# Optimization experiments

Measured on AMD Instinct MI355X. Metric: run time of the kernel, lower is better.

Reference implementation:

```python
import jax, jax.numpy as jnp
import numpy as np
import math

S, B, D, H = 2048, 4, 1024, 16
DH = D // H

def setup_inputs() -> dict:
    key = jax.random.key(0)
    ks = jax.random.split(key, 6)
    x = jax.random.normal(ks[0], (S, B, D), dtype=jnp.float32)
    # causal additive mask (finite large negative for numerical safety)
    i = jnp.arange(S)
    attn_mask = jnp.where(i[None, :] > i[:, None], jnp.float32(-1e9), jnp.float32(0.0))
    beta = jnp.zeros((H,), dtype=jnp.float32)  # per-head log-scale, init 0 -> exp=1
    xav = math.sqrt(6.0 / (D + D))  # xavier_uniform bound
    Wq = jax.random.uniform(ks[1], (D, D), minval=-xav, maxval=xav, dtype=jnp.float32)
    Wk = jax.random.uniform(ks[2], (D, D), minval=-xav, maxval=xav, dtype=jnp.float32)
    Wv = jax.random.uniform(ks[3], (D, D), minval=-xav, maxval=xav, dtype=jnp.float32)
    Wo = jax.random.uniform(ks[4], (D, D), minval=-xav, maxval=xav, dtype=jnp.float32)
    z = jnp.zeros((D,), dtype=jnp.float32)
    return {"x": x, "attn_mask": attn_mask, "beta": beta,
            "Wq": Wq, "bq": z, "Wk": Wk, "bk": z, "Wv": Wv, "bv": z, "Wo": Wo, "bo": z}

def reference(x, attn_mask, beta, Wq, bq, Wk, bk, Wv, bv, Wo, bo):
    s, b, d = x.shape
    h, dh = H, DH
    q = x @ Wq.T + bq  # (s, b, d)
    k = x @ Wk.T + bk
    v = x @ Wv.T + bv
    # attn_sink: append zero key/value token, pad mask with a zero column
    k = jnp.concatenate([k, jnp.zeros((1, b, d), k.dtype)], axis=0)  # (s+1, b, d)
    v = jnp.concatenate([v, jnp.zeros((1, b, d), v.dtype)], axis=0)
    mask = jnp.pad(attn_mask, ((0, 0), (0, 1)))  # (s, s+1)
    t = s + 1
    # split heads: (seq, b, h, dh) -> (b, h, seq, dh)
    qh = q.reshape(s, b, h, dh).transpose(1, 2, 0, 3)
    kh = k.reshape(t, b, h, dh).transpose(1, 2, 0, 3)
    vh = v.reshape(t, b, h, dh).transpose(1, 2, 0, 3)
    scale = (jnp.exp(beta) * math.sqrt(dh))[None, :, None, None]
    qh = qh / scale
    scores = jnp.einsum('bhsd,bhtd->bhst', qh, kh) + mask[None, None]
    w = jax.nn.softmax(scores, axis=-1)
    out = jnp.einsum('bhst,bhtd->bhsd', w, vh)  # (b, h, s, dh)
    out = out.transpose(2, 0, 1, 3).reshape(s, b, d)
    return out @ Wo.T + bo
```

## Files before the change

### kernel.cpp

```cpp
#include <hip/hip_runtime.h>
#include <hip/hip_bf16.h>
#include <math.h>

#define S_LEN   2048
#define BATCH   4
#define DMODEL  1024
#define NHEAD   16
#define DHEAD   64
#define MROWS   (S_LEN * BATCH)

typedef __bf16 bf16;
typedef __bf16 bf16x8 __attribute__((ext_vector_type(8)));
typedef __bf16 bf16x4 __attribute__((ext_vector_type(4)));
typedef short  short4_t __attribute__((ext_vector_type(4)));
typedef float  f32x4  __attribute__((ext_vector_type(4)));

#define LOG2E 1.4426950408889634f

#define AS1C(p) (const __attribute__((address_space(1))) void*)(p)
#define AS3(p)  (__attribute__((address_space(3))) void*)(p)


__global__ __launch_bounds__(256) void cast_all(const float* __restrict__ x,
                                                const float* __restrict__ wq,
                                                const float* __restrict__ wk,
                                                const float* __restrict__ wv,
                                                const float* __restrict__ wo,
                                                bf16* __restrict__ xb,
                                                bf16* __restrict__ wqkv,
                                                bf16* __restrict__ wob) {
    const int i = blockIdx.x * 256 + threadIdx.x;
    constexpr int NX8 = MROWS * DMODEL / 8;
    constexpr int NW8 = DMODEL * DMODEL / 8;
    const float* src;
    bf16* dst;
    int k;
    if (i < NX8) {
        src = x; dst = xb; k = i;
    } else {
        const int j   = i - NX8;
        const int seg = j >> 17;
        k = j & (NW8 - 1);
        if (seg == 0)      { src = wq; dst = wqkv; }
        else if (seg == 1) { src = wk; dst = wqkv + (size_t)DMODEL * DMODEL; }
        else if (seg == 2) { src = wv; dst = wqkv + (size_t)2 * DMODEL * DMODEL; }
        else               { src = wo; dst = wob; }
    }
    const float4* p = (const float4*)src;
    float4 a = p[(size_t)k * 2], b = p[(size_t)k * 2 + 1];
    bf16x8 o;
    o[0] = (bf16)a.x; o[1] = (bf16)a.y; o[2] = (bf16)a.z; o[3] = (bf16)a.w;
    o[4] = (bf16)b.x; o[5] = (bf16)b.y; o[6] = (bf16)b.z; o[7] = (bf16)b.w;
    *(bf16x8*)(dst + (size_t)k * 8) = o;
}

__global__ __launch_bounds__(512, 6) void qkv_gemm(const bf16* __restrict__ A,
                                                   const bf16* __restrict__ W,
                                                   const float* __restrict__ bq,
                                                   const float* __restrict__ bk,
                                                   const float* __restrict__ bv,
                                                   const float* __restrict__ beta,
                                                   bf16* __restrict__ Qo,
                                                   bf16* __restrict__ Kp,
                                                   bf16* __restrict__ Vp) {
    constexpr int BK = 32;
    constexpr int NT = DMODEL / BK;
    __shared__ __align__(16) bf16 sA[3][128 * BK];
    __shared__ __align__(16) bf16 sB[3][128 * BK];
    const int t    = threadIdx.x;
    const int lane = t & 63;
    const int wave = t >> 6;
    const int wr   = wave >> 2;
    const int wc   = wave & 3;
    const int lq   = lane & 15;
    const int lg   = lane >> 4;
    const int bn   = blockIdx.x * 128;
    const int bm   = blockIdx.y * 128;

    const int schunk = (lane & 3) ^ ((lane >> 3) & 3);
    const bf16* ApS = A + (size_t)(bm + wave * 16 + (lane >> 2)) * DMODEL + schunk * 8;
    const bf16* WpS = W + (size_t)(bn + wave * 16 + (lane >> 2)) * DMODEL + schunk * 8;
    const int koff = (lg ^ ((lq >> 1) & 3)) * 8;
    f32x4 acc[4][2] = {};

#define QSTG(si_, ko_)                                                                   \
    __builtin_amdgcn_global_load_lds(AS1C(ApS + (ko_)), AS3(&sA[si_][wave * 512]), 16, 0, 0); \
    __builtin_amdgcn_global_load_lds(AS1C(WpS + (ko_)), AS3(&sB[si_][wave * 512]), 16, 0, 0);

    QSTG(0, 0)
    QSTG(1, BK)
    asm volatile("s_waitcnt vmcnt(2)\n\ts_barrier" ::: "memory");

    int bi = 0, si = 2, st = 2;
    for (int tt = 0; tt < NT; ++tt) {
        QSTG(si, (size_t)st * BK)
        const bf16* At = sA[bi];
        const bf16* Bt = sB[bi];
        bf16x8 bf0 = *(const bf16x8*)&Bt[(wc * 32 +      lq) * BK + koff];
        bf16x8 bf1 = *(const bf16x8*)&Bt[(wc * 32 + 16 + lq) * BK + koff];
        bf16x8 af[4];
#pragma unroll
        for (int mt = 0; mt < 4; mt++)
            af[mt] = *(const bf16x8*)&At[(wr * 64 + mt * 16 + lq) * BK + koff];
        __builtin_amdgcn_s_setprio(1);
#pragma unroll
        for (int mt = 0; mt < 4; mt++) {
            acc[mt][0] = __builtin_amdgcn_mfma_f32_16x16x32_bf16(af[mt], bf0, acc[mt][0], 0, 0, 0);
            acc[mt][1] = __builtin_amdgcn_mfma_f32_16x16x32_bf16(af[mt], bf1, acc[mt][1], 0, 0, 0);
        }
        __builtin_amdgcn_s_setprio(0);
        asm volatile("s_waitcnt vmcnt(2)\n\ts_barrier" ::: "memory");
        bi = (bi == 2) ? 0 : bi + 1;
        si = (si == 2) ? 0 : si + 1;
        st = (st == NT - 1) ? 0 : st + 1;
    }
#undef QSTG

    const int seg = blockIdx.x >> 3;
    const int bnl = (blockIdx.x & 7) * 128;
    const float* bias = (seg == 0) ? bq : (seg == 1) ? bk : bv;

    if (seg == 0) {
#pragma unroll
        for (int nt = 0; nt < 2; nt++) {
            const int col = bnl + wc * 32 + nt * 16 + lq;
            const float bvv = bias[col];
            const float sc = LOG2E / (__expf(beta[col >> 6]) * 8.0f);
#pragma unroll
            for (int mt = 0; mt < 4; mt++) {
                const int row = bm + wr * 64 + mt * 16 + lg * 4;
#pragma unroll
                for (int r = 0; r < 4; r++) {
                    float v = (acc[mt][nt][r] + bvv) * sc;
                    Qo[(size_t)(row + r) * DMODEL + col] = (bf16)v;
                }
            }
        }
    } else {
        bf16* out = (seg == 1) ? Kp : Vp;
#pragma unroll
        for (int mt = 0; mt < 4; mt++) {
            const int F   = bm + wr * 64 + mt * 16;
            const int S0X = F >> 2;
            const int T   = S0X >> 4;
            const int sl  = (S0X & 15) + lg;
#pragma unroll
            for (int nt = 0; nt < 2; nt++) {
                const int col = bnl + wc * 32 + nt * 16 + lq;
                const int h   = col >> 6;
                const int dh  = col & 63;
                const float bvv = bias[col];
#pragma unroll
                for (int r = 0; r < 4; r++) {
                    float v = acc[mt][nt][r] + bvv;
                    size_t addr;
                    if (seg == 1) {
                        addr = ((size_t)((r * 16 + h) * 128 + T)) * 1024
                             + (dh >> 5) * 512
                             + (sl + 16 * ((dh >> 3) & 3)) * 8
                             + (dh & 7);
                    } else {
                        addr = ((size_t)((r * 16 + h) * 128 + T)) * 1024
                             + (dh >> 4) * 256 + ((dh & 15) + 16 * (sl >> 2)) * 4
                             + (sl & 3);
                    }
                    out[addr] = (bf16)v;
                }
            }
        }
    }
}

__global__ __launch_bounds__(256, 3) void gemm_out(const bf16* __restrict__ A,
                                                   const bf16* __restrict__ W,
                                                   const float* __restrict__ bias,
                                                   float* __restrict__ C) {
    constexpr int BK = 32;
    constexpr int NTILES = DMODEL / BK;
    __shared__ __align__(16) bf16 sA[3][128 * BK];
    __shared__ __align__(16) bf16 sB[3][128 * BK];

    const int t    = threadIdx.x;
    const int lane = t & 63;
    const int wave = t >> 6;
    const int wr   = wave >> 1;
    const int wc   = wave & 1;
    const int lq   = lane & 15;
    const int lg   = lane >> 4;

    const int bid = (int)blockIdx.x + 8 * (int)blockIdx.y;
    const int swz = (bid & 7) * 64 + (bid >> 3);
    const int bn  = (swz & 7) * 128;
    const int bm  = (swz >> 3) * 128;

    const int schunk = (lane & 3) ^ ((lane >> 3) & 3);
    const bf16* ApS = A + (size_t)(bm + wave * 32 + (lane >> 2)) * DMODEL + schunk * 8;
    const bf16* WpS = W + (size_t)(bn + wave * 32 + (lane >> 2)) * DMODEL + schunk * 8;
    const int koff = (lg ^ ((lq >> 1) & 3)) * 8;

    f32x4 acc[4][4] = {};

#define OSTAGE(si_, ko_)                                                                              \
    __builtin_amdgcn_global_load_lds(AS1C(ApS + (ko_)),               AS3(&sA[si_][(wave*32 +  0)*BK]), 16,0,0); \
    __builtin_amdgcn_global_load_lds(AS1C(ApS + 16*DMODEL + (ko_)),   AS3(&sA[si_][(wave*32 + 16)*BK]), 16,0,0); \
    __builtin_amdgcn_global_load_lds(AS1C(WpS + (ko_)),               AS3(&sB[si_][(wave*32 +  0)*BK]), 16,0,0); \
    __builtin_amdgcn_global_load_lds(AS1C(WpS + 16*DMODEL + (ko_)),   AS3(&sB[si_][(wave*32 + 16)*BK]), 16,0,0);

    OSTAGE(0, 0)
    OSTAGE(1, BK)
    asm volatile("s_waitcnt vmcnt(4)\n\ts_barrier" ::: "memory");

    int bi = 0, si = 2, st = 2;
    for (int tt = 0; tt < NTILES; ++tt) {
        OSTAGE(si, (size_t)st * BK)
        const bf16* At = sA[bi];
        const bf16* Bt = sB[bi];
        bf16x8 bfr[4], af[4];
#pragma unroll
        for (int nt = 0; nt < 4; nt++)
            bfr[nt] = *(const bf16x8*)&Bt[(wc * 64 + nt * 16 + lq) * BK + koff];
#pragma unroll
        for (int mt = 0; mt < 4; mt++)
            af[mt] = *(const bf16x8*)&At[(wr * 64 + mt * 16 + lq) * BK + koff];
        __builtin_amdgcn_s_setprio(1);
#pragma unroll
        for (int mt = 0; mt < 4; mt++)
#pragma unroll
            for (int nt = 0; nt < 4; nt++)
                acc[mt][nt] = __builtin_amdgcn_mfma_f32_16x16x32_bf16(af[mt], bfr[nt], acc[mt][nt], 0, 0, 0);
        __builtin_amdgcn_s_setprio(0);
        asm volatile("s_waitcnt vmcnt(4)\n\ts_barrier" ::: "memory");
        bi = (bi == 2) ? 0 : bi + 1;
        si = (si == 2) ? 0 : si + 1;
        st = (st == NTILES - 1) ? 0 : st + 1;
    }
#undef OSTAGE

#pragma unroll
    for (int nt = 0; nt < 4; nt++) {
        const int col = bn + wc * 64 + nt * 16 + lq;
        const float bvv = bias[col];
#pragma unroll
        for (int mt = 0; mt < 4; mt++) {
            const int row = bm + wr * 64 + mt * 16 + lg * 4;
#pragma unroll
            for (int r = 0; r < 4; r++)
                C[(size_t)(row + r) * DMODEL + col] = acc[mt][nt][r] + bvv;
        }
    }
}

__global__ __launch_bounds__(256, 3) void attn_kernel(const bf16* __restrict__ Q,
                                                      const bf16* __restrict__ Kp,
                                                      const bf16* __restrict__ Vp,
                                                      bf16* __restrict__ O) {
    __shared__ __align__(16) float sO[64 * 65];
    __shared__ __align__(16) float sL[256];

    const int t    = threadIdx.x;
    const int lane = t & 63;
    const int wave = t >> 6;
    const int lq = lane & 15;
    const int lg = lane >> 4;

    const int bid = (int)blockIdx.x + 16 * ((int)blockIdx.y + 16 * (int)blockIdx.z);
    const int swz = (bid & 7) * 128 + (bid >> 3);
    const int idx = swz & 15;
    const int h   = (swz >> 4) & 15;
    const int b   = swz >> 8;

    const bf16* Kb = Kp + (size_t)(b * NHEAD + h) * 131072;
    const bf16* Vb = Vp + (size_t)(b * NHEAD + h) * 131072;

#pragma clang loop unroll(disable)
    for (int pass = 0; pass < 2; ++pass) {
        const int qi = (pass == 0) ? (31 - idx) : idx;
        const int qb = qi * 64;

        bf16x8 qf[4][2];
#pragma unroll
        for (int nt = 0; nt < 4; nt++)
#pragma unroll
            for (int kc = 0; kc < 2; kc++)
                qf[nt][kc] = *(const bf16x8*)
                    &Q[((size_t)(qb + nt * 16 + lq) * BATCH + b) * DMODEL + h * DHEAD + kc * 32 + lg * 8];

        f32x4 o_acc[4][4] = {};
        float l_lane[4] = {0.f, 0.f, 0.f, 0.f};

        bf16x8 kc0 = *(const bf16x8*)(Kb + (size_t)wave * 1024 + lane * 8);
        bf16x8 kc1 = *(const bf16x8*)(Kb + (size_t)wave * 1024 + 512 + lane * 8);
        bf16x4 vc0 = *(const bf16x4*)(Vb + (size_t)wave * 1024 +   0 + lane * 4);
        bf16x4 vc1 = *(const bf16x4*)(Vb + (size_t)wave * 1024 + 256 + lane * 4);
        bf16x4 vc2 = *(const bf16x4*)(Vb + (size_t)wave * 1024 + 512 + lane * 4);
        bf16x4 vc3 = *(const bf16x4*)(Vb + (size_t)wave * 1024 + 768 + lane * 4);

        for (int kt = 0; kt <= qi; kt++) {
            const int tn = ((kt < qi) ? (kt + 1) : 0) * 4 + wave;
            const bf16* Kn = Kb + (size_t)tn * 1024;
            const bf16* Vn = Vb + (size_t)tn * 1024;
            bf16x8 kn0 = *(const bf16x8*)(Kn + lane * 8);
            bf16x8 kn1 = *(const bf16x8*)(Kn + 512 + lane * 8);
            bf16x4 vn0 = *(const bf16x4*)(Vn +   0 + lane * 4);
            bf16x4 vn1 = *(const bf16x4*)(Vn + 256 + lane * 4);
            bf16x4 vn2 = *(const bf16x4*)(Vn + 512 + lane * 4);
            bf16x4 vn3 = *(const bf16x4*)(Vn + 768 + lane * 4);

            f32x4 st[4];
            __builtin_amdgcn_s_setprio(1);
#pragma unroll
            for (int nt = 0; nt < 4; nt++) {
                f32x4 a = {};
                a = __builtin_amdgcn_mfma_f32_16x16x32_bf16(kc0, qf[nt][0], a, 0, 0, 0);
                a = __builtin_amdgcn_mfma_f32_16x16x32_bf16(kc1, qf[nt][1], a, 0, 0, 0);
                st[nt] = a;
            }
            __builtin_amdgcn_s_setprio(0);

            if (kt == qi) {
#pragma unroll
                for (int nt = 0; nt < 4; nt++)
#pragma unroll
                    for (int r = 0; r < 4; r++)
                        if (wave * 16 + lg * 4 + r > nt * 16 + lq) st[nt][r] = -1e30f;
            }

            short4_t pf[4];
#pragma unroll
            for (int nt = 0; nt < 4; nt++) {
                float p0 = __builtin_amdgcn_exp2f(st[nt][0]);
                float p1 = __builtin_amdgcn_exp2f(st[nt][1]);
                float p2 = __builtin_amdgcn_exp2f(st[nt][2]);
                float p3 = __builtin_amdgcn_exp2f(st[nt][3]);
                l_lane[nt] += (p0 + p1) + (p2 + p3);
                bf16x4 pv;
                pv[0] = (bf16)p0; pv[1] = (bf16)p1; pv[2] = (bf16)p2; pv[3] = (bf16)p3;
                pf[nt] = __builtin_bit_cast(short4_t, pv);
            }

            short4_t va0 = __builtin_bit_cast(short4_t, vc0);
            short4_t va1 = __builtin_bit_cast(short4_t, vc1);
            short4_t va2 = __builtin_bit_cast(short4_t, vc2);
            short4_t va3 = __builtin_bit_cast(short4_t, vc3);
            __builtin_amdgcn_s_setprio(1);
#pragma unroll
            for (int nt = 0; nt < 4; nt++) {
                o_acc[0][nt] = __builtin_amdgcn_mfma_f32_16x16x16bf16_1k(va0, pf[nt], o_acc[0][nt], 0, 0, 0);
                o_acc[1][nt] = __builtin_amdgcn_mfma_f32_16x16x16bf16_1k(va1, pf[nt], o_acc[1][nt], 0, 0, 0);
                o_acc[2][nt] = __builtin_amdgcn_mfma_f32_16x16x16bf16_1k(va2, pf[nt], o_acc[2][nt], 0, 0, 0);
                o_acc[3][nt] = __builtin_amdgcn_mfma_f32_16x16x16bf16_1k(va3, pf[nt], o_acc[3][nt], 0, 0, 0);
            }
            __builtin_amdgcn_s_setprio(0);

            kc0 = kn0; kc1 = kn1;
            vc0 = vn0; vc1 = vn1; vc2 = vn2; vc3 = vn3;
        }

#pragma unroll
        for (int nt = 0; nt < 4; nt++) {
            float v = l_lane[nt];
            v += __shfl_xor(v, 16);
            v += __shfl_xor(v, 32);
            if (lg == 0) sL[wave * 64 + nt * 16 + lq] = v;
        }

#pragma unroll
        for (int rd = 0; rd < 4; rd++) {
#pragma unroll
            for (int dtc = 0; dtc < 4; dtc++) {
                if (((wave + rd) & 3) == dtc) {
                    if (rd == 0) {
#pragma unroll
                        for (int nt = 0; nt < 4; nt++)
#pragma unroll
                            for (int r = 0; r < 4; r++)
                                sO[(dtc * 16 + lg * 4 + r) * 65 + nt * 16 + lq] = o_acc[dtc][nt][r];
                    } else {
#pragma unroll
                        for (int nt = 0; nt < 4; nt++)
#pragma unroll
                            for (int r = 0; r < 4; r++)
                                sO[(dtc * 16 + lg * 4 + r) * 65 + nt * 16 + lq] += o_acc[dtc][nt][r];
                    }
                }
            }
            __syncthreads();
        }

        const int dt = wave;
        float rec[4];
#pragma unroll
        for (int nt = 0; nt < 4; nt++) {
            float lt = 1.0f + sL[nt * 16 + lq] + sL[64 + nt * 16 + lq]
                     + sL[128 + nt * 16 + lq] + sL[192 + nt * 16 + lq];
            rec[nt] = 1.0f / lt;
        }
#pragma unroll
        for (int nt = 0; nt < 4; nt++) {
            bf16x4 ov;
#pragma unroll
            for (int r = 0; r < 4; r++)
                ov[r] = (bf16)(sO[(dt * 16 + lg * 4 + r) * 65 + nt * 16 + lq] * rec[nt]);
            *(bf16x4*)&O[((size_t)(qb + nt * 16 + lq) * BATCH + b) * DMODEL + h * DHEAD + dt * 16 + lg * 4] = ov;
        }

        __syncthreads();
    }
}

extern "C" void kernel_launch(void* const* d_in, const int* in_sizes, int n_in,
                              void* d_out, int out_size, void* d_ws, size_t ws_size,
                              hipStream_t stream) {
    const float* x    = (const float*)d_in[0];
    const float* beta = (const float*)d_in[2];
    const float* Wq   = (const float*)d_in[3];
    const float* bq   = (const float*)d_in[4];
    const float* Wk   = (const float*)d_in[5];
    const float* bk   = (const float*)d_in[6];
    const float* Wv   = (const float*)d_in[7];
    const float* bv   = (const float*)d_in[8];
    const float* Wo   = (const float*)d_in[9];
    const float* bo   = (const float*)d_in[10];
    float* out = (float*)d_out;

    char* ws = (char*)d_ws;
    size_t off = 0;
    auto alloc = [&](size_t bytes) -> void* {
        void* p = ws + off;
        off += (bytes + 255) & ~(size_t)255;
        return p;
    };
    const size_t xbytes = (size_t)MROWS * DMODEL * sizeof(bf16);
    const size_t wbytes = (size_t)DMODEL * DMODEL * sizeof(bf16);
    bf16* xb   = (bf16*)alloc(xbytes);
    bf16* wqkv = (bf16*)alloc(3 * wbytes);
    bf16* wob  = (bf16*)alloc(wbytes);
    bf16* qws  = (bf16*)alloc(xbytes);
    bf16* kpb  = (bf16*)alloc(xbytes);
    bf16* vpb  = (bf16*)alloc(xbytes);
    bf16* aob  = (bf16*)alloc(xbytes);

    constexpr int NX8 = MROWS * DMODEL / 8;
    constexpr int NW8 = DMODEL * DMODEL / 8;
    cast_all<<<(NX8 + 4 * NW8) / 256, 256, 0, stream>>>(x, Wq, Wk, Wv, Wo, xb, wqkv, wob);

    dim3 qgrid(3 * DMODEL / 128, MROWS / 128);
    qkv_gemm<<<qgrid, 512, 0, stream>>>(xb, wqkv, bq, bk, bv, beta, qws, kpb, vpb);

    dim3 agrid(S_LEN / 128, NHEAD, BATCH);
    attn_kernel<<<agrid, 256, 0, stream>>>(qws, kpb, vpb, aob);

    dim3 ogrid(DMODEL / 128, MROWS / 128);
    gemm_out<<<ogrid, 256, 0, stream>>>(aob, wob, bo, out);
}
```

Before: 274.7 us.

## Split attention into one query tile per block and stage Q in LDS

```diff
diff --git a/kernel.cpp b/kernel.cpp
--- a/kernel.cpp
+++ b/kernel.cpp
@@ -250,12 +250,13 @@
     }
 }
 
-__global__ __launch_bounds__(256, 3) void attn_kernel(const bf16* __restrict__ Q,
+__global__ __launch_bounds__(256, 4) void attn_kernel(const bf16* __restrict__ Q,
                                                       const bf16* __restrict__ Kp,
                                                       const bf16* __restrict__ Vp,
                                                       bf16* __restrict__ O) {
     __shared__ __align__(16) float sO[64 * 65];
     __shared__ __align__(16) float sL[256];
+    __shared__ __align__(16) bf16  sQ[4096];
 
     const int t    = threadIdx.x;
     const int lane = t & 63;
@@ -263,148 +264,149 @@
     const int lq = lane & 15;
     const int lg = lane >> 4;
 
-    const int bid = (int)blockIdx.x + 16 * ((int)blockIdx.y + 16 * (int)blockIdx.z);
-    const int swz = (bid & 7) * 128 + (bid >> 3);
-    const int idx = swz & 15;
-    const int h   = (swz >> 4) & 15;
-    const int b   = swz >> 8;
+    const int bid = (int)blockIdx.x + 32 * ((int)blockIdx.y + 16 * (int)blockIdx.z);
+    const int swz = (bid & 7) * 256 + (bid >> 3);
+    const int qi  = 31 - (swz & 31);
+    const int h   = (swz >> 5) & 15;
+    const int b   = swz >> 9;
+    const int qb  = qi * 64;
 
     const bf16* Kb = Kp + (size_t)(b * NHEAD + h) * 131072;
     const bf16* Vb = Vp + (size_t)(b * NHEAD + h) * 131072;
 
-#pragma clang loop unroll(disable)
-    for (int pass = 0; pass < 2; ++pass) {
-        const int qi = (pass == 0) ? (31 - idx) : idx;
-        const int qb = qi * 64;
-
-        bf16x8 qf[4][2];
-#pragma unroll
-        for (int nt = 0; nt < 4; nt++)
-#pragma unroll
-            for (int kc = 0; kc < 2; kc++)
-                qf[nt][kc] = *(const bf16x8*)
-                    &Q[((size_t)(qb + nt * 16 + lq) * BATCH + b) * DMODEL + h * DHEAD + kc * 32 + lg * 8];
-
-        f32x4 o_acc[4][4] = {};
-        float l_lane[4] = {0.f, 0.f, 0.f, 0.f};
-
-        bf16x8 kc0 = *(const bf16x8*)(Kb + (size_t)wave * 1024 + lane * 8);
-        bf16x8 kc1 = *(const bf16x8*)(Kb + (size_t)wave * 1024 + 512 + lane * 8);
-        bf16x4 vc0 = *(const bf16x4*)(Vb + (size_t)wave * 1024 +   0 + lane * 4);
-        bf16x4 vc1 = *(const bf16x4*)(Vb + (size_t)wave * 1024 + 256 + lane * 4);
-        bf16x4 vc2 = *(const bf16x4*)(Vb + (size_t)wave * 1024 + 512 + lane * 4);
-        bf16x4 vc3 = *(const bf16x4*)(Vb + (size_t)wave * 1024 + 768 + lane * 4);
-
-        for (int kt = 0; kt <= qi; kt++) {
-            const int tn = ((kt < qi) ? (kt + 1) : 0) * 4 + wave;
-            const bf16* Kn = Kb + (size_t)tn * 1024;
-            const bf16* Vn = Vb + (size_t)tn * 1024;
-            bf16x8 kn0 = *(const bf16x8*)(Kn + lane * 8);
-            bf16x8 kn1 = *(const bf16x8*)(Kn + 512 + lane * 8);
-            bf16x4 vn0 = *(const bf16x4*)(Vn +   0 + lane * 4);
-            bf16x4 vn1 = *(const bf16x4*)(Vn + 256 + lane * 4);
-            bf16x4 vn2 = *(const bf16x4*)(Vn + 512 + lane * 4);
-            bf16x4 vn3 = *(const bf16x4*)(Vn + 768 + lane * 4);
-
-            f32x4 st[4];
-            __builtin_amdgcn_s_setprio(1);
-#pragma unroll
-            for (int nt = 0; nt < 4; nt++) {
-                f32x4 a = {};
-                a = __builtin_amdgcn_mfma_f32_16x16x32_bf16(kc0, qf[nt][0], a, 0, 0, 0);
-                a = __builtin_amdgcn_mfma_f32_16x16x32_bf16(kc1, qf[nt][1], a, 0, 0, 0);
-                st[nt] = a;
-            }
-            __builtin_amdgcn_s_setprio(0);
-
-            if (kt == qi) {
-#pragma unroll
-                for (int nt = 0; nt < 4; nt++)
-#pragma unroll
-                    for (int r = 0; r < 4; r++)
-                        if (wave * 16 + lg * 4 + r > nt * 16 + lq) st[nt][r] = -1e30f;
-            }
-
-            short4_t pf[4];
-#pragma unroll
-            for (int nt = 0; nt < 4; nt++) {
-                float p0 = __builtin_amdgcn_exp2f(st[nt][0]);
-                float p1 = __builtin_amdgcn_exp2f(st[nt][1]);
-                float p2 = __builtin_amdgcn_exp2f(st[nt][2]);
-                float p3 = __builtin_amdgcn_exp2f(st[nt][3]);
-                l_lane[nt] += (p0 + p1) + (p2 + p3);
-                bf16x4 pv;
-                pv[0] = (bf16)p0; pv[1] = (bf16)p1; pv[2] = (bf16)p2; pv[3] = (bf16)p3;
-                pf[nt] = __builtin_bit_cast(short4_t, pv);
-            }
-
-            short4_t va0 = __builtin_bit_cast(short4_t, vc0);
-            short4_t va1 = __builtin_bit_cast(short4_t, vc1);
-            short4_t va2 = __builtin_bit_cast(short4_t, vc2);
-            short4_t va3 = __builtin_bit_cast(short4_t, vc3);
-            __builtin_amdgcn_s_setprio(1);
-#pragma unroll
-            for (int nt = 0; nt < 4; nt++) {
-                o_acc[0][nt] = __builtin_amdgcn_mfma_f32_16x16x16bf16_1k(va0, pf[nt], o_acc[0][nt], 0, 0, 0);
-                o_acc[1][nt] = __builtin_amdgcn_mfma_f32_16x16x16bf16_1k(va1, pf[nt], o_acc[1][nt], 0, 0, 0);
-                o_acc[2][nt] = __builtin_amdgcn_mfma_f32_16x16x16bf16_1k(va2, pf[nt], o_acc[2][nt], 0, 0, 0);
-                o_acc[3][nt] = __builtin_amdgcn_mfma_f32_16x16x16bf16_1k(va3, pf[nt], o_acc[3][nt], 0, 0, 0);
-            }
-            __builtin_amdgcn_s_setprio(0);
-
-            kc0 = kn0; kc1 = kn1;
-            vc0 = vn0; vc1 = vn1; vc2 = vn2; vc3 = vn3;
-        }
-
+    {
+        const int rw  = wave * 8 + (lane >> 3);
+        const int lch = (lane & 7) ^ (lane >> 3);
+        const bf16* q0 = Q + ((size_t)(qb + rw) * BATCH + b) * DMODEL + h * DHEAD + lch * 8;
+        const bf16* q1 = Q + ((size_t)(qb + 32 + rw) * BATCH + b) * DMODEL + h * DHEAD + lch * 8;
+        __builtin_amdgcn_global_load_lds(AS1C(q0), AS3(&sQ[wave * 512]),        16, 0, 0);
+        __builtin_amdgcn_global_load_lds(AS1C(q1), AS3(&sQ[2048 + wave * 512]), 16, 0, 0);
+    }
+
+    const int a0 = lq * 64 + ((0 + lg) ^ (lq & 7)) * 8;
+    const int a1 = lq * 64 + ((4 + lg) ^ (lq & 7)) * 8;
+
+    f32x4 o_acc[4][4] = {};
+    float l_lane[4] = {0.f, 0.f, 0.f, 0.f};
+
+    bf16x8 kc0 = *(const bf16x8*)(Kb + (size_t)wave * 1024 + lane * 8);
+    bf16x8 kc1 = *(const bf16x8*)(Kb + (size_t)wave * 1024 + 512 + lane * 8);
+    bf16x4 vc0 = *(const bf16x4*)(Vb + (size_t)wave * 1024 +   0 + lane * 4);
+    bf16x4 vc1 = *(const bf16x4*)(Vb + (size_t)wave * 1024 + 256 + lane * 4);
+    bf16x4 vc2 = *(const bf16x4*)(Vb + (size_t)wave * 1024 + 512 + lane * 4);
+    bf16x4 vc3 = *(const bf16x4*)(Vb + (size_t)wave * 1024 + 768 + lane * 4);
+
+    asm volatile("s_waitcnt vmcnt(0)\n\ts_barrier" ::: "memory");
+
+    for (int kt = 0; kt <= qi; kt++) {
+        const int tn = ((kt < qi) ? (kt + 1) : 0) * 4 + wave;
+        const bf16* Kn = Kb + (size_t)tn * 1024;
+        const bf16* Vn = Vb + (size_t)tn * 1024;
+        bf16x8 kn0 = *(const bf16x8*)(Kn + lane * 8);
+        bf16x8 kn1 = *(const bf16x8*)(Kn + 512 + lane * 8);
+        bf16x4 vn0 = *(const bf16x4*)(Vn +   0 + lane * 4);
+        bf16x4 vn1 = *(const bf16x4*)(Vn + 256 + lane * 4);
+        bf16x4 vn2 = *(const bf16x4*)(Vn + 512 + lane * 4);
+        bf16x4 vn3 = *(const bf16x4*)(Vn + 768 + lane * 4);
+
+        f32x4 st[4];
+        __builtin_amdgcn_s_setprio(1);
 #pragma unroll
         for (int nt = 0; nt < 4; nt++) {
-            float v = l_lane[nt];
-            v += __shfl_xor(v, 16);
-            v += __shfl_xor(v, 32);
-            if (lg == 0) sL[wave * 64 + nt * 16 + lq] = v;
-        }
-
-#pragma unroll
-        for (int rd = 0; rd < 4; rd++) {
-#pragma unroll
-            for (int dtc = 0; dtc < 4; dtc++) {
-                if (((wave + rd) & 3) == dtc) {
-                    if (rd == 0) {
-#pragma unroll
-                        for (int nt = 0; nt < 4; nt++)
-#pragma unroll
-                            for (int r = 0; r < 4; r++)
-                                sO[(dtc * 16 + lg * 4 + r) * 65 + nt * 16 + lq] = o_acc[dtc][nt][r];
-                    } else {
-#pragma unroll
-                        for (int nt = 0; nt < 4; nt++)
-#pragma unroll
-                            for (int r = 0; r < 4; r++)
-                                sO[(dtc * 16 + lg * 4 + r) * 65 + nt * 16 + lq] += o_acc[dtc][nt][r];
-                    }
+            bf16x8 q0 = *(const bf16x8*)&sQ[nt * 1024 + a0];
+            bf16x8 q1 = *(const bf16x8*)&sQ[nt * 1024 + a1];
+            f32x4 a = {};
+            a = __builtin_amdgcn_mfma_f32_16x16x32_bf16(kc0, q0, a, 0, 0, 0);
+            a = __builtin_amdgcn_mfma_f32_16x16x32_bf16(kc1, q1, a, 0, 0, 0);
+            st[nt] = a;
+        }
+        __builtin_amdgcn_s_setprio(0);
+
+        if (kt == qi) {
+#pragma unroll
+            for (int nt = 0; nt < 4; nt++)
+#pragma unroll
+                for (int r = 0; r < 4; r++)
+                    if (wave * 16 + lg * 4 + r > nt * 16 + lq) st[nt][r] = -1e30f;
+        }
+
+        short4_t pf[4];
+#pragma unroll
+        for (int nt = 0; nt < 4; nt++) {
+            float p0 = __builtin_amdgcn_exp2f(st[nt][0]);
+            float p1 = __builtin_amdgcn_exp2f(st[nt][1]);
+            float p2 = __builtin_amdgcn_exp2f(st[nt][2]);
+            float p3 = __builtin_amdgcn_exp2f(st[nt][3]);
+            l_lane[nt] += (p0 + p1) + (p2 + p3);
+            bf16x4 pv;
+            pv[0] = (bf16)p0; pv[1] = (bf16)p1; pv[2] = (bf16)p2; pv[3] = (bf16)p3;
+            pf[nt] = __builtin_bit_cast(short4_t, pv);
+        }
+
+        short4_t va0 = __builtin_bit_cast(short4_t, vc0);
+        short4_t va1 = __builtin_bit_cast(short4_t, vc1);
+        short4_t va2 = __builtin_bit_cast(short4_t, vc2);
+        short4_t va3 = __builtin_bit_cast(short4_t, vc3);
+        __builtin_amdgcn_s_setprio(1);
+#pragma unroll
+        for (int nt = 0; nt < 4; nt++) {
+            o_acc[0][nt] = __builtin_amdgcn_mfma_f32_16x16x16bf16_1k(va0, pf[nt], o_acc[0][nt], 0, 0, 0);
+            o_acc[1][nt] = __builtin_amdgcn_mfma_f32_16x16x16bf16_1k(va1, pf[nt], o_acc[1][nt], 0, 0, 0);
+            o_acc[2][nt] = __builtin_amdgcn_mfma_f32_16x16x16bf16_1k(va2, pf[nt], o_acc[2][nt], 0, 0, 0);
+            o_acc[3][nt] = __builtin_amdgcn_mfma_f32_16x16x16bf16_1k(va3, pf[nt], o_acc[3][nt], 0, 0, 0);
+        }
+        __builtin_amdgcn_s_setprio(0);
+
+        kc0 = kn0; kc1 = kn1;
+        vc0 = vn0; vc1 = vn1; vc2 = vn2; vc3 = vn3;
+    }
+
+#pragma unroll
+    for (int nt = 0; nt < 4; nt++) {
+        float v = l_lane[nt];
+        v += __shfl_xor(v, 16);
+        v += __shfl_xor(v, 32);
+        if (lg == 0) sL[wave * 64 + nt * 16 + lq] = v;
+    }
+
+#pragma unroll
+    for (int rd = 0; rd < 4; rd++) {
+#pragma unroll
+        for (int dtc = 0; dtc < 4; dtc++) {
+            if (((wave + rd) & 3) == dtc) {
+                if (rd == 0) {
+#pragma unroll
+                    for (int nt = 0; nt < 4; nt++)
+#pragma unroll
+                        for (int r = 0; r < 4; r++)
+                            sO[(dtc * 16 + lg * 4 + r) * 65 + nt * 16 + lq] = o_acc[dtc][nt][r];
+                } else {
+#pragma unroll
+                    for (int nt = 0; nt < 4; nt++)
+#pragma unroll
+                        for (int r = 0; r < 4; r++)
+                            sO[(dtc * 16 + lg * 4 + r) * 65 + nt * 16 + lq] += o_acc[dtc][nt][r];
                 }
             }
-            __syncthreads();
-        }
-
-        const int dt = wave;
-        float rec[4];
-#pragma unroll
-        for (int nt = 0; nt < 4; nt++) {
-            float lt = 1.0f + sL[nt * 16 + lq] + sL[64 + nt * 16 + lq]
-                     + sL[128 + nt * 16 + lq] + sL[192 + nt * 16 + lq];
-            rec[nt] = 1.0f / lt;
-        }
-#pragma unroll
-        for (int nt = 0; nt < 4; nt++) {
-            bf16x4 ov;
-#pragma unroll
-            for (int r = 0; r < 4; r++)
-                ov[r] = (bf16)(sO[(dt * 16 + lg * 4 + r) * 65 + nt * 16 + lq] * rec[nt]);
-            *(bf16x4*)&O[((size_t)(qb + nt * 16 + lq) * BATCH + b) * DMODEL + h * DHEAD + dt * 16 + lg * 4] = ov;
-        }
-
+        }
         __syncthreads();
+    }
+
+    const int dt = wave;
+    float rec[4];
+#pragma unroll
+    for (int nt = 0; nt < 4; nt++) {
+        float lt = 1.0f + sL[nt * 16 + lq] + sL[64 + nt * 16 + lq]
+                 + sL[128 + nt * 16 + lq] + sL[192 + nt * 16 + lq];
+        rec[nt] = 1.0f / lt;
+    }
+#pragma unroll
+    for (int nt = 0; nt < 4; nt++) {
+        bf16x4 ov;
+#pragma unroll
+        for (int r = 0; r < 4; r++)
+            ov[r] = (bf16)(sO[(dt * 16 + lg * 4 + r) * 65 + nt * 16 + lq] * rec[nt]);
+        *(bf16x4*)&O[((size_t)(qb + nt * 16 + lq) * BATCH + b) * DMODEL + h * DHEAD + dt * 16 + lg * 4] = ov;
     }
 }
 
@@ -447,7 +449,7 @@
     dim3 qgrid(3 * DMODEL / 128, MROWS / 128);
     qkv_gemm<<<qgrid, 512, 0, stream>>>(xb, wqkv, bq, bk, bv, beta, qws, kpb, vpb);
 
-    dim3 agrid(S_LEN / 128, NHEAD, BATCH);
+    dim3 agrid(S_LEN / 64, NHEAD, BATCH);
     attn_kernel<<<agrid, 256, 0, stream>>>(qws, kpb, vpb, aob);
 
     dim3 ogrid(DMODEL / 128, MROWS / 128);
```

After: 418.9 us. 1.53x slower.
